# Kernel optimization log

Measured on AMD Instinct MI355X. Metric: run time of the kernel, lower is better.

Reference implementation:

```python
import jax, jax.numpy as jnp
import numpy as np

B, LQ, LK, DIM = 2, 2048, 2048, 1024
HEADS, DH = 8, 64
INNER = HEADS * DH  # 512


def setup_inputs() -> dict:
    key = jax.random.key(0)
    ks = jax.random.split(key, 7)
    x = jax.random.normal(ks[0], (B, LQ, DIM), dtype=jnp.float32)
    y = jax.random.normal(ks[1], (B, LK, DIM), dtype=jnp.float32)
    # binary mask, 1 => masked (gets -1e9 added)
    mask = jax.random.randint(ks[2], (B, LQ, LK), 0, 2).astype(jnp.float32)
    s = 0.02
    Wq = jax.random.normal(ks[3], (INNER, DIM), dtype=jnp.float32) * s
    Wk = jax.random.normal(ks[4], (INNER, DIM), dtype=jnp.float32) * s
    Wv = jax.random.normal(ks[5], (INNER, DIM), dtype=jnp.float32) * s
    Wo = jax.random.normal(ks[6], (DIM, INNER), dtype=jnp.float32) * s
    return {"x": x, "y": y, "mask": mask, "Wq": Wq, "Wk": Wk, "Wv": Wv, "Wo": Wo}


def reference(x, y, mask, Wq, Wk, Wv, Wo):
    scale = DH ** -0.5
    # projections (Linear without bias: x @ W.T)
    q = (x @ Wq.T) * scale            # [B, LQ, INNER]
    k = y @ Wk.T                      # [B, LK, INNER]
    v = y @ Wv.T                      # [B, LK, INNER]
    # split into heads (torch.split along last dim == reshape to [.., H, DH])
    q = q.reshape(B, LQ, HEADS, DH)
    k = k.reshape(B, LK, HEADS, DH)
    v = v.reshape(B, LK, HEADS, DH)
    # per-head QK^T + additive mask*-1e9, softmax over keys, then V
    scores = jnp.einsum('bqhd,bkhd->bhqk', q, k) + mask[:, None, :, :] * (-1e9)
    attn = jax.nn.softmax(scores, axis=-1)
    out = jnp.einsum('bhqk,bkhd->bqhd', attn, v).reshape(B, LQ, INNER)
    return out @ Wo.T                 # [B, LQ, DIM]
```

## Files before the change

kernel.cpp:

```cpp
#include <hip/hip_runtime.h>
#include <hip/hip_bf16.h>
#include <stdint.h>

#define BATCH 2
#define LQ 2048
#define LK 2048
#define DIM 1024
#define HEADS 8
#define DH 64
#define INNER 512

typedef __attribute__((ext_vector_type(8))) short short8;
typedef __attribute__((ext_vector_type(4))) float f32x4;

__device__ __forceinline__ float bf2f(unsigned short u) {
    union { unsigned int i; float f; } v;
    v.i = ((unsigned int)u) << 16;
    return v.f;
}
__device__ __forceinline__ unsigned short f2bf(float f) {
    __hip_bfloat16 h = __float2bfloat16(f);
    return *reinterpret_cast<unsigned short*>(&h);
}
__device__ __forceinline__ float fexp2(float x) {
#if __has_builtin(__builtin_amdgcn_exp2f)
    return __builtin_amdgcn_exp2f(x);
#else
    return __expf(x * 0.69314718056f);
#endif
}
__device__ __forceinline__ void stc(unsigned short* C, size_t i, float v) { C[i] = f2bf(v); }
__device__ __forceinline__ void stc(float* C, size_t i, float v) { C[i] = v; }

__device__ __forceinline__ unsigned cvtpk_bf16(float lo, float hi) {
    unsigned r;
    asm("v_cvt_pk_bf16_f32 %0, %1, %2" : "=v"(r) : "v"(lo), "v"(hi));
    return r;
}
__device__ __forceinline__ void perm32swap(unsigned& a, unsigned& b) {
#if __has_builtin(__builtin_amdgcn_permlane32_swap)
    auto r = __builtin_amdgcn_permlane32_swap(a, b, false, false);
    a = r[0]; b = r[1];
#else
    asm volatile("v_permlane32_swap_b32 %0, %1" : "+v"(a), "+v"(b));
#endif
}
__device__ __forceinline__ void perm16swap(unsigned& a, unsigned& b) {
#if __has_builtin(__builtin_amdgcn_permlane16_swap)
    auto r = __builtin_amdgcn_permlane16_swap(a, b, false, false);
    a = r[0]; b = r[1];
#else
    asm volatile("v_permlane16_swap_b32 %0, %1" : "+v"(a), "+v"(b));
#endif
}

typedef __attribute__((address_space(1))) const unsigned int gu32;
typedef __attribute__((address_space(3))) unsigned int lu32;
__device__ __forceinline__ void gload16(const void* g, void* l) {
    __builtin_amdgcn_global_load_lds((gu32*)g, (lu32*)l, 16, 0, 0);
}

__global__ __launch_bounds__(256) void prep(
    const float* __restrict__ x,  const float* __restrict__ y,
    const float* __restrict__ wq, const float* __restrict__ wk,
    const float* __restrict__ wv, const float* __restrict__ wo,
    const float* __restrict__ mask,
    unsigned short* __restrict__ xb,  unsigned short* __restrict__ yb,
    unsigned short* __restrict__ wqb, unsigned short* __restrict__ wkb,
    unsigned short* __restrict__ wvb, unsigned short* __restrict__ wob,
    unsigned long long* __restrict__ mbits)
{
    if (blockIdx.y == 6) {
        const int wid = blockIdx.x * 4 + (threadIdx.x >> 6);
        const int lane = threadIdx.x & 63;
        for (int task = wid; task < BATCH * LQ * 8; task += 4096) {
            int row = task >> 3, g = task & 7;
            const float* mp = mask + (size_t)row * LK + g * 256;
            unsigned long long* ob = mbits + (size_t)row * (LK / 64) + g * 4;
            float v0 = mp[0 * 64 + lane];
            float v1 = mp[1 * 64 + lane];
            float v2 = mp[2 * 64 + lane];
            float v3 = mp[3 * 64 + lane];
            unsigned long long b0 = __ballot(v0 > 0.5f);
            unsigned long long b1 = __ballot(v1 > 0.5f);
            unsigned long long b2 = __ballot(v2 > 0.5f);
            unsigned long long b3 = __ballot(v3 > 0.5f);
            if (lane == 0) { ob[0] = b0; ob[1] = b1; ob[2] = b2; ob[3] = b3; }
        }
        return;
    }
    const float* src; unsigned short* dst; int n4;
    switch (blockIdx.y) {
        case 0: src = x;  dst = xb;  n4 = (BATCH * LQ * DIM) / 4; break;
        case 1: src = y;  dst = yb;  n4 = (BATCH * LK * DIM) / 4; break;
        case 2: src = wq; dst = wqb; n4 = (INNER * DIM) / 4; break;
        case 3: src = wk; dst = wkb; n4 = (INNER * DIM) / 4; break;
        case 4: src = wv; dst = wvb; n4 = (INNER * DIM) / 4; break;
        default: src = wo; dst = wob; n4 = (INNER * DIM) / 4; break;
    }
    const int stride = gridDim.x * 256;
    for (int i = blockIdx.x * 256 + threadIdx.x; i < n4; i += stride) {
        float4 f = ((const float4*)src)[i];
        ushort4 u;
        u.x = f2bf(f.x); u.y = f2bf(f.y); u.z = f2bf(f.z); u.w = f2bf(f.w);
        ((ushort4*)dst)[i] = u;
    }
}

template <int IM, int JN, int WR, int WC, typename TC, int EPI>
__device__ __forceinline__ void gemm_body(
    const unsigned short* __restrict__ A,
    const unsigned short* __restrict__ W,
    TC* __restrict__ C,
    int K, int N, float scale,
    unsigned short* SH)
{
    constexpr int THREADS = WR * WC * 64;
    constexpr int BM = WR * IM * 16;
    constexpr int BN = WC * JN * 16;
    constexpr int ACH = BM * 8;
    constexpr int BCH = BN * 8;
    constexpr int AUS = BM * 64;
    constexpr int BUS = BN * 64;

    unsigned short* As = SH;
    unsigned short* Bs = SH + 2 * AUS;

    const int tid = threadIdx.x;
    const int m0 = blockIdx.x * BM;
    const int n0 = blockIdx.y * BN;
    const int w = tid >> 6, lane = tid & 63;
    const int q4 = lane >> 4, l16 = lane & 15;
    const int wm = (w / WC) * (IM * 16), wn = (w % WC) * (JN * 16);
    const int sw = l16 & 7;

    f32x4 acc[IM][JN] = {};

#pragma unroll
    for (int i = 0; i < ACH / THREADS; ++i) {
        int s = tid + i * THREADS;
        int r = s >> 3, ch = (s & 7) ^ (r & 7);
        gload16(A + (size_t)(m0 + r) * K + ch * 8, As + (size_t)s * 8);
    }
#pragma unroll
    for (int i = 0; i < BCH / THREADS; ++i) {
        int s = tid + i * THREADS;
        int r = s >> 3, ch = (s & 7) ^ (r & 7);
        gload16(W + (size_t)(n0 + r) * K + ch * 8, Bs + (size_t)s * 8);
    }
    __syncthreads();

    const int nt = K / 64;
    for (int t = 0; t < nt; ++t) {
        const int curA = (t & 1) * AUS;
        const int curB = (t & 1) * BUS;
        if (t + 1 < nt) {
            int kk = (t + 1) * 64;
            const int nxtA = AUS - curA, nxtB = BUS - curB;
#pragma unroll
            for (int i = 0; i < ACH / THREADS; ++i) {
                int s = tid + i * THREADS;
                int r = s >> 3, ch = (s & 7) ^ (r & 7);
                gload16(A + (size_t)(m0 + r) * K + kk + ch * 8, As + nxtA + (size_t)s * 8);
            }
#pragma unroll
            for (int i = 0; i < BCH / THREADS; ++i) {
                int s = tid + i * THREADS;
                int r = s >> 3, ch = (s & 7) ^ (r & 7);
                gload16(W + (size_t)(n0 + r) * K + kk + ch * 8, Bs + nxtB + (size_t)s * 8);
            }
        }

#pragma unroll
        for (int ks = 0; ks < 2; ++ks) {
            const int kq = ((ks * 4 + q4) ^ sw) * 8;
            short8 a[IM], b[JN];
#pragma unroll
            for (int i = 0; i < IM; ++i)
                a[i] = *(const short8*)(As + curA + (wm + i * 16 + l16) * 64 + kq);
#pragma unroll
            for (int j = 0; j < JN; ++j)
                b[j] = *(const short8*)(Bs + curB + (wn + j * 16 + l16) * 64 + kq);
#pragma unroll
            for (int i = 0; i < IM; ++i)
#pragma unroll
                for (int j = 0; j < JN; ++j)
                    acc[i][j] = __builtin_amdgcn_mfma_f32_16x16x32_bf16(
                        a[i], b[j], acc[i][j], 0, 0, 0);
        }
        __syncthreads();
    }

    if (EPI == 0) {
#pragma unroll
        for (int i = 0; i < IM; ++i)
#pragma unroll
            for (int j = 0; j < JN; ++j)
#pragma unroll
                for (int r = 0; r < 4; ++r) {
                    int row = m0 + wm + i * 16 + q4 * 4 + r;
                    int col = n0 + wn + j * 16 + l16;
                    stc(C, (size_t)row * N + col, acc[i][j][r] * scale);
                }
    } else {
        constexpr int KW = IM * 16;
        constexpr int DW = JN * 16;
        constexpr int TPS = KW + 8;
        unsigned short* TP = SH + w * (DW * TPS);
#pragma unroll
        for (int i = 0; i < IM; ++i)
#pragma unroll
            for (int j = 0; j < JN; ++j) {
                ushort4 u;
                u.x = f2bf(acc[i][j][0]); u.y = f2bf(acc[i][j][1]);
                u.z = f2bf(acc[i][j][2]); u.w = f2bf(acc[i][j][3]);
                *(ushort4*)(TP + (j * 16 + l16) * TPS + i * 16 + q4 * 4) = u;
            }
        const int keyflat = m0 + wm;
        const int bb = keyflat >> 11, key0 = keyflat & (LK - 1);
        const int hh = (n0 + wn) >> 6;
        const int dlow = (n0 + wn) & 63;
        constexpr int RCH = KW / 8;
        constexpr int NCH = DW * RCH;
#pragma unroll
        for (int p = 0; p < NCH / 64; ++p) {
            int c = p * 64 + lane;
            int dl = c / RCH, kc = c % RCH;
            uint4 v = *(const uint4*)(TP + dl * TPS + kc * 8);
            *(uint4*)((unsigned short*)C +
                ((size_t)((bb * HEADS + hh) * DH + dlow + dl)) * LK + key0 + kc * 8) = v;
        }
    }
}

#define QSCALE 0.18033688011112042f

__global__ __launch_bounds__(512) void proj_qkv(
    const unsigned short* __restrict__ xb, const unsigned short* __restrict__ yb,
    const unsigned short* __restrict__ wqb, const unsigned short* __restrict__ wkb,
    const unsigned short* __restrict__ wvb,
    unsigned short* __restrict__ qb, unsigned short* __restrict__ kb,
    unsigned short* __restrict__ vt)
{
    __shared__ __align__(16) unsigned short SH[4 * 128 * 64];
    const int z = blockIdx.z;
    const unsigned short* A = (z == 0) ? xb : yb;
    const unsigned short* W = (z == 0) ? wqb : (z == 1) ? wkb : wvb;
    if (z == 2)
        gemm_body<4, 2, 2, 4, unsigned short, 1>(A, W, vt, DIM, INNER, 1.0f, SH);
    else
        gemm_body<4, 2, 2, 4, unsigned short, 0>(A, W, (z == 0) ? qb : kb, DIM, INNER,
                                                 (z == 0) ? QSCALE : 1.0f, SH);
}

__global__ __launch_bounds__(512) void gemm_out(
    const unsigned short* __restrict__ A,
    const unsigned short* __restrict__ W,
    float* __restrict__ C)
{
    __shared__ __align__(16) unsigned short SH[4 * 128 * 64];
    gemm_body<4, 2, 2, 4, float, 0>(A, W, C, INNER, DIM, 1.0f, SH);
}

#define AT_SLOT (64 * 64)

__global__ __launch_bounds__(512, 4) void attn_mfma(
    const unsigned short* __restrict__ Q,
    const unsigned short* __restrict__ Kb,
    const unsigned short* __restrict__ Vt,
    const unsigned long long* __restrict__ Mb,
    unsigned short* __restrict__ O)
{
    __shared__ __align__(16) unsigned short Ks[4 * AT_SLOT];
    __shared__ __align__(16) unsigned short Vs[4 * AT_SLOT];

    const int tid = threadIdx.x;
    const int q0 = blockIdx.x * 64;
    const int h = blockIdx.y, b = blockIdx.z;
    const int w = tid >> 6, lane = tid & 63;
    const int g = w & 3;
    const int par = w >> 2;
    const int q4 = lane >> 4, l16 = lane & 15;
    const int sw = l16 & 7;

    short8 qf[2];
    {
        const unsigned short* qp =
            Q + (size_t)(b * LQ + q0 + g * 16 + l16) * INNER + h * DH + q4 * 8;
        qf[0] = *(const short8*)(qp);
        qf[1] = *(const short8*)(qp + 32);
    }

    f32x4 o[4] = {};
    float lacc = 0.f;

    const unsigned short* kbase = Kb + (size_t)(b * LK) * INNER + h * DH;
    const unsigned short* vbase = Vt + (size_t)((b * HEADS + h) * DH) * LK;
    const unsigned long long* mrow =
        Mb + (size_t)(b * LQ + q0 + g * 16 + l16) * (LK / 64);

    const int rr = tid >> 3;
    const int ch = (tid & 7) ^ (rr & 7);

#pragma unroll
    for (int tn = 0; tn < 2; ++tn) {
        gload16(kbase + (size_t)(tn * 64 + rr) * INNER + ch * 8,
                Ks + tn * AT_SLOT + (size_t)tid * 8);
        gload16(vbase + (size_t)rr * LK + tn * 64 + ch * 8,
                Vs + tn * AT_SLOT + (size_t)tid * 8);
    }
    __syncthreads();

    const int NR = LK / 128;
    for (int rd = 0; rd < NR; ++rd) {
        if (rd + 1 < NR) {
#pragma unroll
            for (int i = 0; i < 2; ++i) {
                const int tn = 2 * rd + 2 + i;
                const int sl = tn & 3;
                gload16(kbase + (size_t)(tn * 64 + rr) * INNER + ch * 8,
                        Ks + sl * AT_SLOT + (size_t)tid * 8);
                gload16(vbase + (size_t)rr * LK + tn * 64 + ch * 8,
                        Vs + sl * AT_SLOT + (size_t)tid * 8);
            }
        }
        const int t = 2 * rd + par;
        const int cur = (t & 3) * AT_SLOT;

        f32x4 s[4];
#pragma unroll
        for (int j = 0; j < 4; ++j) {
            s[j] = f32x4{0.f, 0.f, 0.f, 0.f};
#pragma unroll
            for (int ks = 0; ks < 2; ++ks) {
                short8 kf = *(const short8*)(Ks + cur + (j * 16 + l16) * 64
                                             + (((ks * 4 + q4) ^ sw) * 8));
                s[j] = __builtin_amdgcn_mfma_f32_16x16x32_bf16(kf, qf[ks], s[j], 0, 0, 0);
            }
        }

        unsigned long long bsh = mrow[t] >> (q4 * 4);
        unsigned pk[8];
#pragma unroll
        for (int j = 0; j < 4; ++j) {
            unsigned nib = (unsigned)(bsh >> (16 * j)) & 0xFu;
            float p0 = (nib & 1u) ? 0.f : fexp2(s[j][0]);
            float p1 = (nib & 2u) ? 0.f : fexp2(s[j][1]);
            float p2 = (nib & 4u) ? 0.f : fexp2(s[j][2]);
            float p3 = (nib & 8u) ? 0.f : fexp2(s[j][3]);
            lacc += (p0 + p1) + (p2 + p3);
            pk[2 * j]     = cvtpk_bf16(p0, p1);
            pk[2 * j + 1] = cvtpk_bf16(p2, p3);
        }

        short8 pf[2];
#pragma unroll
        for (int ks = 0; ks < 2; ++ks) {
            unsigned a0 = pk[4 * ks + 0], b0 = pk[4 * ks + 2];
            unsigned a1 = pk[4 * ks + 1], b1 = pk[4 * ks + 3];
            perm32swap(a0, b0); perm16swap(a0, b0);
            perm32swap(a1, b1); perm16swap(a1, b1);
            union { unsigned u[4]; short8 s8; } up;
            up.u[0] = a0; up.u[1] = a1; up.u[2] = b0; up.u[3] = b1;
            pf[ks] = up.s8;
        }

#pragma unroll
        for (int ks = 0; ks < 2; ++ks) {
#pragma unroll
            for (int dd = 0; dd < 4; ++dd) {
                short8 vf = *(const short8*)(Vs + cur + (dd * 16 + l16) * 64
                                             + (((ks * 4 + q4) ^ sw) * 8));
                o[dd] = __builtin_amdgcn_mfma_f32_16x16x32_bf16(vf, pf[ks], o[dd], 0, 0, 0);
            }
        }
        __syncthreads();
    }

    float* xch = (float*)Ks;
    if (par) {
        float* d = xch + (size_t)(g * 64 + lane) * 17;
#pragma unroll
        for (int dd = 0; dd < 4; ++dd)
#pragma unroll
            for (int r2 = 0; r2 < 4; ++r2) d[dd * 4 + r2] = o[dd][r2];
        d[16] = lacc;
    }
    __syncthreads();
    if (!par) {
        const float* d = xch + (size_t)(g * 64 + lane) * 17;
#pragma unroll
        for (int dd = 0; dd < 4; ++dd)
#pragma unroll
            for (int r2 = 0; r2 < 4; ++r2) o[dd][r2] += d[dd * 4 + r2];
        lacc += d[16];

        lacc += __shfl_xor(lacc, 16);
        lacc += __shfl_xor(lacc, 32);
        const float inv = 1.0f / lacc;

        unsigned short* orow =
            O + (size_t)(b * LQ + q0 + g * 16 + l16) * INNER + h * DH + q4 * 4;
#pragma unroll
        for (int dd = 0; dd < 4; ++dd) {
            ushort4 u;
            u.x = f2bf(o[dd][0] * inv); u.y = f2bf(o[dd][1] * inv);
            u.z = f2bf(o[dd][2] * inv); u.w = f2bf(o[dd][3] * inv);
            *(ushort4*)(orow + dd * 16) = u;
        }
    }
}

extern "C" void kernel_launch(void* const* d_in, const int* in_sizes, int n_in,
                              void* d_out, int out_size, void* d_ws, size_t ws_size,
                              hipStream_t stream) {
    const float* x    = (const float*)d_in[0];
    const float* y    = (const float*)d_in[1];
    const float* mask = (const float*)d_in[2];
    const float* Wq   = (const float*)d_in[3];
    const float* Wk   = (const float*)d_in[4];
    const float* Wv   = (const float*)d_in[5];
    const float* Wo   = (const float*)d_in[6];
    float* out = (float*)d_out;

    const size_t NX = (size_t)BATCH * LQ * DIM;
    const size_t NS = (size_t)BATCH * LQ * INNER;
    const size_t NW = (size_t)INNER * DIM;
    unsigned short* xb  = (unsigned short*)d_ws;
    unsigned short* yb  = xb + NX;
    unsigned short* qb  = yb + NX;
    unsigned short* kb  = qb + NS;
    unsigned short* vt  = kb + NS;
    unsigned short* wqb = vt + NS;
    unsigned short* wkb = wqb + NW;
    unsigned short* wvb = wkb + NW;
    unsigned short* wob = wvb + NW;
    unsigned long long* mbits = (unsigned long long*)(wob + NW);
    unsigned short* ao  = xb;

    dim3 blk(256);
    prep<<<dim3(1024, 7), blk, 0, stream>>>(
        x, y, Wq, Wk, Wv, Wo, mask, xb, yb, wqb, wkb, wvb, wob, mbits);
    proj_qkv<<<dim3(4096 / 128, INNER / 128, 3), dim3(512), 0, stream>>>(
        xb, yb, wqb, wkb, wvb, qb, kb, vt);
    attn_mfma<<<dim3(LQ / 64, HEADS, BATCH), dim3(512), 0, stream>>>(
        qb, kb, vt, mbits, ao);
    gemm_out<<<dim3(4096 / 128, DIM / 128), dim3(512), 0, stream>>>(ao, wob, out);
}
```

Measured before the change: 171.8 us.

## Load K/V MFMA fragments directly from global memory instead of LDS staging

The attention kernel drops its shared-memory ring buffer for K and V tiles and its per-iteration barriers. Each wave now reads its MFMA fragments straight from global memory, relying on L2 and L1 to serve the reuse across the 4 query-group waves. The grid is also flattened to 1D with head as the fastest-varying index, so neighbouring blocks share K/V for the same batch more closely in time. The trade is more global and cache traffic and exposed load latency in exchange for no LDS writes, no sync stalls and lower LDS pressure.

```diff
diff --git a/kernel.cpp b/kernel.cpp
--- a/kernel.cpp
+++ b/kernel.cpp
@@ -262,8 +262,6 @@
     gemm_body<4, 2, 2, 4, float, 0>(A, W, C, INNER, DIM, 1.0f, SH);
 }
 
-#define AT_SLOT (64 * 64)
-
 __global__ __launch_bounds__(512, 4) void attn_mfma(
     const unsigned short* __restrict__ Q,
     const unsigned short* __restrict__ Kb,
@@ -271,17 +269,18 @@
     const unsigned long long* __restrict__ Mb,
     unsigned short* __restrict__ O)
 {
-    __shared__ __align__(16) unsigned short Ks[4 * AT_SLOT];
-    __shared__ __align__(16) unsigned short Vs[4 * AT_SLOT];
+    __shared__ __align__(16) float xch[4 * 64 * 17];
 
     const int tid = threadIdx.x;
-    const int q0 = blockIdx.x * 64;
-    const int h = blockIdx.y, b = blockIdx.z;
+    const int L = blockIdx.x;
+    const int h = L & 7;
+    const int jj = L >> 3;
+    const int b = jj >> 5;
+    const int q0 = (jj & 31) * 64;
     const int w = tid >> 6, lane = tid & 63;
     const int g = w & 3;
     const int par = w >> 2;
     const int q4 = lane >> 4, l16 = lane & 15;
-    const int sw = l16 & 7;
 
     short8 qf[2];
     {
@@ -294,49 +293,29 @@
     f32x4 o[4] = {};
     float lacc = 0.f;
 
-    const unsigned short* kbase = Kb + (size_t)(b * LK) * INNER + h * DH;
-    const unsigned short* vbase = Vt + (size_t)((b * HEADS + h) * DH) * LK;
+    const unsigned short* kfrag =
+        Kb + (size_t)(b * LK + l16) * INNER + h * DH + q4 * 8;
+    const unsigned short* vfrag =
+        Vt + (size_t)((b * HEADS + h) * DH + l16) * LK + q4 * 8;
     const unsigned long long* mrow =
         Mb + (size_t)(b * LQ + q0 + g * 16 + l16) * (LK / 64);
 
-    const int rr = tid >> 3;
-    const int ch = (tid & 7) ^ (rr & 7);
-
-#pragma unroll
-    for (int tn = 0; tn < 2; ++tn) {
-        gload16(kbase + (size_t)(tn * 64 + rr) * INNER + ch * 8,
-                Ks + tn * AT_SLOT + (size_t)tid * 8);
-        gload16(vbase + (size_t)rr * LK + tn * 64 + ch * 8,
-                Vs + tn * AT_SLOT + (size_t)tid * 8);
-    }
-    __syncthreads();
-
-    const int NR = LK / 128;
-    for (int rd = 0; rd < NR; ++rd) {
-        if (rd + 1 < NR) {
-#pragma unroll
-            for (int i = 0; i < 2; ++i) {
-                const int tn = 2 * rd + 2 + i;
-                const int sl = tn & 3;
-                gload16(kbase + (size_t)(tn * 64 + rr) * INNER + ch * 8,
-                        Ks + sl * AT_SLOT + (size_t)tid * 8);
-                gload16(vbase + (size_t)rr * LK + tn * 64 + ch * 8,
-                        Vs + sl * AT_SLOT + (size_t)tid * 8);
-            }
-        }
-        const int t = 2 * rd + par;
-        const int cur = (t & 3) * AT_SLOT;
-
+    const int NT = LK / 64;
+    for (int t = par; t < NT; t += 2) {
         f32x4 s[4];
+        short8 kf[4][2];
+#pragma unroll
+        for (int j = 0; j < 4; ++j)
+#pragma unroll
+            for (int ks = 0; ks < 2; ++ks)
+                kf[j][ks] = *(const short8*)(kfrag
+                    + (size_t)(t * 64 + j * 16) * INNER + ks * 32);
 #pragma unroll
         for (int j = 0; j < 4; ++j) {
             s[j] = f32x4{0.f, 0.f, 0.f, 0.f};
 #pragma unroll
-            for (int ks = 0; ks < 2; ++ks) {
-                short8 kf = *(const short8*)(Ks + cur + (j * 16 + l16) * 64
-                                             + (((ks * 4 + q4) ^ sw) * 8));
-                s[j] = __builtin_amdgcn_mfma_f32_16x16x32_bf16(kf, qf[ks], s[j], 0, 0, 0);
-            }
+            for (int ks = 0; ks < 2; ++ks)
+                s[j] = __builtin_amdgcn_mfma_f32_16x16x32_bf16(kf[j][ks], qf[ks], s[j], 0, 0, 0);
         }
 
         unsigned long long bsh = mrow[t] >> (q4 * 4);
@@ -367,17 +346,17 @@
 
 #pragma unroll
         for (int ks = 0; ks < 2; ++ks) {
-#pragma unroll
-            for (int dd = 0; dd < 4; ++dd) {
-                short8 vf = *(const short8*)(Vs + cur + (dd * 16 + l16) * 64
-                                             + (((ks * 4 + q4) ^ sw) * 8));
-                o[dd] = __builtin_amdgcn_mfma_f32_16x16x32_bf16(vf, pf[ks], o[dd], 0, 0, 0);
-            }
-        }
-        __syncthreads();
-    }
-
-    float* xch = (float*)Ks;
+            short8 vf[4];
+#pragma unroll
+            for (int dd = 0; dd < 4; ++dd)
+                vf[dd] = *(const short8*)(vfrag
+                    + (size_t)(dd * 16) * LK + t * 64 + ks * 32);
+#pragma unroll
+            for (int dd = 0; dd < 4; ++dd)
+                o[dd] = __builtin_amdgcn_mfma_f32_16x16x32_bf16(vf[dd], pf[ks], o[dd], 0, 0, 0);
+        }
+    }
+
     if (par) {
         float* d = xch + (size_t)(g * 64 + lane) * 17;
 #pragma unroll
@@ -443,7 +422,7 @@
         x, y, Wq, Wk, Wv, Wo, mask, xb, yb, wqb, wkb, wvb, wob, mbits);
     proj_qkv<<<dim3(4096 / 128, INNER / 128, 3), dim3(512), 0, stream>>>(
         xb, yb, wqb, wkb, wvb, qb, kb, vt);
-    attn_mfma<<<dim3(LQ / 64, HEADS, BATCH), dim3(512), 0, stream>>>(
+    attn_mfma<<<dim3(512), dim3(512), 0, stream>>>(
         qb, kb, vt, mbits, ao);
     gemm_out<<<dim3(4096 / 128, DIM / 128), dim3(512), 0, stream>>>(ao, wob, out);
 }
```

After: 262.0 us. 52.5% more time.

## Halve attention block to 256 threads, each wave computing two query tiles

Applied to the files above, without the earlier changes.

The attention kernel now runs 4 waves per block instead of 8. Each wave handles two 16-row query groups, so every K and V fragment read from shared memory feeds two MFMAs instead of one. Each thread issues twice as many global-to-LDS loads to fill the same tiles. The aim is to cut LDS read traffic per FLOP and raise MFMA density, at the cost of roughly doubled accumulator registers and fewer waves available to hide latency.

```diff
diff --git a/kernel.cpp b/kernel.cpp
--- a/kernel.cpp
+++ b/kernel.cpp
@@ -264,7 +264,7 @@
 
 #define AT_SLOT (64 * 64)
 
-__global__ __launch_bounds__(512, 4) void attn_mfma(
+__global__ __launch_bounds__(256) void attn_mfma(
     const unsigned short* __restrict__ Q,
     const unsigned short* __restrict__ Kb,
     const unsigned short* __restrict__ Vt,
@@ -278,36 +278,44 @@
     const int q0 = blockIdx.x * 64;
     const int h = blockIdx.y, b = blockIdx.z;
     const int w = tid >> 6, lane = tid & 63;
-    const int g = w & 3;
-    const int par = w >> 2;
+    const int qpos = w & 1;
+    const int par = w >> 1;
     const int q4 = lane >> 4, l16 = lane & 15;
     const int sw = l16 & 7;
 
-    short8 qf[2];
-    {
+    short8 qf[2][2];
+#pragma unroll
+    for (int gg = 0; gg < 2; ++gg) {
         const unsigned short* qp =
-            Q + (size_t)(b * LQ + q0 + g * 16 + l16) * INNER + h * DH + q4 * 8;
-        qf[0] = *(const short8*)(qp);
-        qf[1] = *(const short8*)(qp + 32);
-    }
-
-    f32x4 o[4] = {};
-    float lacc = 0.f;
+            Q + (size_t)(b * LQ + q0 + qpos * 32 + gg * 16 + l16) * INNER + h * DH + q4 * 8;
+        qf[gg][0] = *(const short8*)(qp);
+        qf[gg][1] = *(const short8*)(qp + 32);
+    }
+
+    f32x4 o[2][4] = {};
+    float lacc[2] = {0.f, 0.f};
 
     const unsigned short* kbase = Kb + (size_t)(b * LK) * INNER + h * DH;
     const unsigned short* vbase = Vt + (size_t)((b * HEADS + h) * DH) * LK;
-    const unsigned long long* mrow =
-        Mb + (size_t)(b * LQ + q0 + g * 16 + l16) * (LK / 64);
-
-    const int rr = tid >> 3;
-    const int ch = (tid & 7) ^ (rr & 7);
+    const unsigned long long* mrow[2];
+#pragma unroll
+    for (int gg = 0; gg < 2; ++gg)
+        mrow[gg] = Mb + (size_t)(b * LQ + q0 + qpos * 32 + gg * 16 + l16) * (LK / 64);
+
+    const int r0 = tid >> 3, ch0 = (tid & 7) ^ (r0 & 7);
+    const int st1 = tid + 256;
+    const int r1 = st1 >> 3, ch1 = (st1 & 7) ^ (r1 & 7);
 
 #pragma unroll
     for (int tn = 0; tn < 2; ++tn) {
-        gload16(kbase + (size_t)(tn * 64 + rr) * INNER + ch * 8,
+        gload16(kbase + (size_t)(tn * 64 + r0) * INNER + ch0 * 8,
                 Ks + tn * AT_SLOT + (size_t)tid * 8);
-        gload16(vbase + (size_t)rr * LK + tn * 64 + ch * 8,
+        gload16(kbase + (size_t)(tn * 64 + r1) * INNER + ch1 * 8,
+                Ks + tn * AT_SLOT + (size_t)st1 * 8);
+        gload16(vbase + (size_t)r0 * LK + tn * 64 + ch0 * 8,
                 Vs + tn * AT_SLOT + (size_t)tid * 8);
+        gload16(vbase + (size_t)r1 * LK + tn * 64 + ch1 * 8,
+                Vs + tn * AT_SLOT + (size_t)st1 * 8);
     }
     __syncthreads();
 
@@ -318,51 +326,60 @@
             for (int i = 0; i < 2; ++i) {
                 const int tn = 2 * rd + 2 + i;
                 const int sl = tn & 3;
-                gload16(kbase + (size_t)(tn * 64 + rr) * INNER + ch * 8,
+                const int kn = tn * 64;
+                gload16(kbase + (size_t)(kn + r0) * INNER + ch0 * 8,
                         Ks + sl * AT_SLOT + (size_t)tid * 8);
-                gload16(vbase + (size_t)rr * LK + tn * 64 + ch * 8,
+                gload16(kbase + (size_t)(kn + r1) * INNER + ch1 * 8,
+                        Ks + sl * AT_SLOT + (size_t)st1 * 8);
+                gload16(vbase + (size_t)r0 * LK + kn + ch0 * 8,
                         Vs + sl * AT_SLOT + (size_t)tid * 8);
+                gload16(vbase + (size_t)r1 * LK + kn + ch1 * 8,
+                        Vs + sl * AT_SLOT + (size_t)st1 * 8);
             }
         }
         const int t = 2 * rd + par;
         const int cur = (t & 3) * AT_SLOT;
 
-        f32x4 s[4];
+        f32x4 s[2][4];
 #pragma unroll
         for (int j = 0; j < 4; ++j) {
-            s[j] = f32x4{0.f, 0.f, 0.f, 0.f};
+            s[0][j] = f32x4{0.f, 0.f, 0.f, 0.f};
+            s[1][j] = f32x4{0.f, 0.f, 0.f, 0.f};
 #pragma unroll
             for (int ks = 0; ks < 2; ++ks) {
                 short8 kf = *(const short8*)(Ks + cur + (j * 16 + l16) * 64
                                              + (((ks * 4 + q4) ^ sw) * 8));
-                s[j] = __builtin_amdgcn_mfma_f32_16x16x32_bf16(kf, qf[ks], s[j], 0, 0, 0);
-            }
-        }
-
-        unsigned long long bsh = mrow[t] >> (q4 * 4);
-        unsigned pk[8];
-#pragma unroll
-        for (int j = 0; j < 4; ++j) {
-            unsigned nib = (unsigned)(bsh >> (16 * j)) & 0xFu;
-            float p0 = (nib & 1u) ? 0.f : fexp2(s[j][0]);
-            float p1 = (nib & 2u) ? 0.f : fexp2(s[j][1]);
-            float p2 = (nib & 4u) ? 0.f : fexp2(s[j][2]);
-            float p3 = (nib & 8u) ? 0.f : fexp2(s[j][3]);
-            lacc += (p0 + p1) + (p2 + p3);
-            pk[2 * j]     = cvtpk_bf16(p0, p1);
-            pk[2 * j + 1] = cvtpk_bf16(p2, p3);
-        }
-
-        short8 pf[2];
-#pragma unroll
-        for (int ks = 0; ks < 2; ++ks) {
-            unsigned a0 = pk[4 * ks + 0], b0 = pk[4 * ks + 2];
-            unsigned a1 = pk[4 * ks + 1], b1 = pk[4 * ks + 3];
-            perm32swap(a0, b0); perm16swap(a0, b0);
-            perm32swap(a1, b1); perm16swap(a1, b1);
-            union { unsigned u[4]; short8 s8; } up;
-            up.u[0] = a0; up.u[1] = a1; up.u[2] = b0; up.u[3] = b1;
-            pf[ks] = up.s8;
+                s[0][j] = __builtin_amdgcn_mfma_f32_16x16x32_bf16(kf, qf[0][ks], s[0][j], 0, 0, 0);
+                s[1][j] = __builtin_amdgcn_mfma_f32_16x16x32_bf16(kf, qf[1][ks], s[1][j], 0, 0, 0);
+            }
+        }
+
+        short8 pf[2][2];
+#pragma unroll
+        for (int gg = 0; gg < 2; ++gg) {
+            unsigned long long bsh = mrow[gg][t] >> (q4 * 4);
+            unsigned pk[8];
+#pragma unroll
+            for (int j = 0; j < 4; ++j) {
+                unsigned nib = (unsigned)(bsh >> (16 * j)) & 0xFu;
+                float p0 = (nib & 1u) ? 0.f : fexp2(s[gg][j][0]);
+                float p1 = (nib & 2u) ? 0.f : fexp2(s[gg][j][1]);
+                float p2 = (nib & 4u) ? 0.f : fexp2(s[gg][j][2]);
+                float p3 = (nib & 8u) ? 0.f : fexp2(s[gg][j][3]);
+                lacc[gg] += (p0 + p1) + (p2 + p3);
+                pk[2 * j]     = cvtpk_bf16(p0, p1);
+                pk[2 * j + 1] = cvtpk_bf16(p2, p3);
+            }
+#pragma unroll
+            for (int ks = 0; ks < 2; ++ks) {
+                unsigned a0 = pk[4 * ks + 0], b0 = pk[4 * ks + 2];
+                unsigned a1 = pk[4 * ks + 1], b1 = pk[4 * ks + 3];
+                perm32swap(a0, b0); perm16swap(a0, b0);
+                perm32swap(a1, b1); perm16swap(a1, b1);
+                union { unsigned u[4]; short8 s8; } up;
+                up.u[0] = a0; up.u[1] = a1; up.u[2] = b0; up.u[3] = b1;
+                pf[gg][ks] = up.s8;
+            }
         }
 
 #pragma unroll
@@ -371,7 +388,8 @@
             for (int dd = 0; dd < 4; ++dd) {
                 short8 vf = *(const short8*)(Vs + cur + (dd * 16 + l16) * 64
                                              + (((ks * 4 + q4) ^ sw) * 8));
-                o[dd] = __builtin_amdgcn_mfma_f32_16x16x32_bf16(vf, pf[ks], o[dd], 0, 0, 0);
+                o[0][dd] = __builtin_amdgcn_mfma_f32_16x16x32_bf16(vf, pf[0][ks], o[0][dd], 0, 0, 0);
+                o[1][dd] = __builtin_amdgcn_mfma_f32_16x16x32_bf16(vf, pf[1][ks], o[1][dd], 0, 0, 0);
             }
         }
         __syncthreads();
@@ -379,34 +397,48 @@
 
     float* xch = (float*)Ks;
     if (par) {
-        float* d = xch + (size_t)(g * 64 + lane) * 17;
-#pragma unroll
-        for (int dd = 0; dd < 4; ++dd)
-#pragma unroll
-            for (int r2 = 0; r2 < 4; ++r2) d[dd * 4 + r2] = o[dd][r2];
-        d[16] = lacc;
+        float* d = xch + (size_t)(qpos * 64 + lane) * 35;
+#pragma unroll
+        for (int gg = 0; gg < 2; ++gg) {
+#pragma unroll
+            for (int dd = 0; dd < 4; ++dd)
+#pragma unroll
+                for (int r2 = 0; r2 < 4; ++r2)
+                    d[gg * 16 + dd * 4 + r2] = o[gg][dd][r2];
+            d[32 + gg] = lacc[gg];
+        }
     }
     __syncthreads();
     if (!par) {
-        const float* d = xch + (size_t)(g * 64 + lane) * 17;
-#pragma unroll
-        for (int dd = 0; dd < 4; ++dd)
-#pragma unroll
-            for (int r2 = 0; r2 < 4; ++r2) o[dd][r2] += d[dd * 4 + r2];
-        lacc += d[16];
-
-        lacc += __shfl_xor(lacc, 16);
-        lacc += __shfl_xor(lacc, 32);
-        const float inv = 1.0f / lacc;
-
-        unsigned short* orow =
-            O + (size_t)(b * LQ + q0 + g * 16 + l16) * INNER + h * DH + q4 * 4;
-#pragma unroll
-        for (int dd = 0; dd < 4; ++dd) {
-            ushort4 u;
-            u.x = f2bf(o[dd][0] * inv); u.y = f2bf(o[dd][1] * inv);
-            u.z = f2bf(o[dd][2] * inv); u.w = f2bf(o[dd][3] * inv);
-            *(ushort4*)(orow + dd * 16) = u;
+        const float* d = xch + (size_t)(qpos * 64 + lane) * 35;
+#pragma unroll
+        for (int gg = 0; gg < 2; ++gg) {
+#pragma unroll
+            for (int dd = 0; dd < 4; ++dd)
+#pragma unroll
+                for (int r2 = 0; r2 < 4; ++r2)
+                    o[gg][dd][r2] += d[gg * 16 + dd * 4 + r2];
+            lacc[gg] += d[32 + gg];
+        }
+
+#pragma unroll
+        for (int gg = 0; gg < 2; ++gg) {
+            lacc[gg] += __shfl_xor(lacc[gg], 16);
+            lacc[gg] += __shfl_xor(lacc[gg], 32);
+        }
+
+#pragma unroll
+        for (int gg = 0; gg < 2; ++gg) {
+            const float inv = 1.0f / lacc[gg];
+            unsigned short* orow =
+                O + (size_t)(b * LQ + q0 + qpos * 32 + gg * 16 + l16) * INNER + h * DH + q4 * 4;
+#pragma unroll
+            for (int dd = 0; dd < 4; ++dd) {
+                ushort4 u;
+                u.x = f2bf(o[gg][dd][0] * inv); u.y = f2bf(o[gg][dd][1] * inv);
+                u.z = f2bf(o[gg][dd][2] * inv); u.w = f2bf(o[gg][dd][3] * inv);
+                *(ushort4*)(orow + dd * 16) = u;
+            }
         }
     }
 }
@@ -443,7 +475,7 @@
         x, y, Wq, Wk, Wv, Wo, mask, xb, yb, wqb, wkb, wvb, wob, mbits);
     proj_qkv<<<dim3(4096 / 128, INNER / 128, 3), dim3(512), 0, stream>>>(
         xb, yb, wqb, wkb, wvb, qb, kb, vt);
-    attn_mfma<<<dim3(LQ / 64, HEADS, BATCH), dim3(512), 0, stream>>>(
+    attn_mfma<<<dim3(LQ / 64, HEADS, BATCH), dim3(256), 0, stream>>>(
         qb, kb, vt, mbits, ao);
     gemm_out<<<dim3(4096 / 128, DIM / 128), dim3(512), 0, stream>>>(ao, wob, out);
 }
```

Result: no change. 174.3 us (+1.4%).
